# Performance work log

Hardware: AMD Instinct MI355X
Metric: run time of the kernel (lower is better)

The kernel has to match this reference:

```python
import jax, jax.numpy as jnp
import numpy as np

N, C_IN, H, W = 32, 16, 256, 256
C_OUT, K = 64, 3

def setup_inputs() -> dict:
    key = jax.random.key(0)
    kx, kw, kb = jax.random.split(key, 3)
    x = jax.random.normal(kx, (N, C_IN, H, W), dtype=jnp.float32)
    # PyTorch Conv2d default init: U(-b, b), b = 1/sqrt(fan_in)
    bound = 1.0 / np.sqrt(C_IN * K * K)
    conv_weight = jax.random.uniform(kw, (C_OUT, C_IN, K, K), minval=-bound, maxval=bound, dtype=jnp.float32)
    conv_bias = jax.random.uniform(kb, (C_OUT,), minval=-bound, maxval=bound, dtype=jnp.float32)
    return {"x": x, "conv_weight": conv_weight, "conv_bias": conv_bias}

def reference(x, conv_weight, conv_bias):
    # conv2d, stride=1, padding=0 (VALID), NCHW / OIHW
    y = jax.lax.conv_general_dilated(
        x, conv_weight,
        window_strides=(1, 1), padding="VALID",
        dimension_numbers=("NCHW", "OIHW", "NCHW"))
    y = y + conv_bias[None, :, None, None]
    # min over output channels (keepdim -> 1 channel), then double tanh
    y = jnp.min(y, axis=1, keepdims=True)  # [N,1,OH,OW]
    return jnp.tanh(jnp.tanh(y))
```

## Files before the change

kernel.cpp:

```cpp
#include <hip/hip_runtime.h>

typedef __bf16 bf16x8 __attribute__((ext_vector_type(8)));
typedef unsigned short us8 __attribute__((ext_vector_type(8)));
typedef unsigned short us2 __attribute__((ext_vector_type(2)));
typedef float f32x16 __attribute__((ext_vector_type(16)));

#define N_IMG 32
#define CI 16
#define HH 256
#define WW 256
#define CO 64
#define OHH 254
#define OWW 254
#define RPB 2
#define NBLK_H (OHH / RPB)
#define NBLK (N_IMG * NBLK_H)

#define XS_W 258
#define XS_C 24
#define WP_SHORTS (CO * 160)
#define WS_NEEDED ((size_t)WP_SHORTS * 2)

__device__ __forceinline__ unsigned short f2bf(float f) {
  union { float f; unsigned u; } v; v.f = f;
  return (unsigned short)((v.u + 0x7FFFu + ((v.u >> 16) & 1u)) >> 16);
}

#if defined(__has_builtin)
#if __has_builtin(__builtin_amdgcn_cvt_pk_bf16_f32)
#define HAVE_CVT_PK 1
#endif
#endif

__device__ __forceinline__ us2 cvt2(float a, float b) {
#ifdef HAVE_CVT_PK
  typedef __bf16 bf16x2 __attribute__((ext_vector_type(2)));
  bf16x2 r = __builtin_amdgcn_cvt_pk_bf16_f32(a, b);
  return __builtin_bit_cast(us2, r);
#else
  us2 r; r[0] = f2bf(a); r[1] = f2bf(b); return r;
#endif
}

__device__ __forceinline__ float fast_tanh(float x) {
  float cx = fminf(fmaxf(x, -15.f), 15.f);
  float e = __expf(2.f * cx);
  return (e - 1.f) / (e + 1.f);
}

__global__ void prep_w(const float* __restrict__ wg, const float* __restrict__ bg,
                       unsigned short* __restrict__ wp) {
  int idx = blockIdx.x * 256 + threadIdx.x;
  if (idx >= WP_SHORTS) return;
  int oc = idx / 160;
  int k = idx - oc * 160;
  int tap = k >> 4, ci = k & 15;
  float v;
  if (tap < 9)      v = wg[oc * 144 + ci * 9 + tap];
  else if (ci == 0) v = bg[oc];
  else              v = 0.f;
  wp[idx] = f2bf(v);
}

__global__ __launch_bounds__(256, 3)
void conv_fused(const float* __restrict__ xg, const unsigned short* __restrict__ wp,
                float* __restrict__ out) {
  __shared__ __align__(16) unsigned short xs[(RPB + 2) * XS_W * XS_C];
  const int t = threadIdx.x;
  const int n = blockIdx.x / NBLK_H;
  const int oh0 = (blockIdx.x - n * NBLK_H) * RPB;

  {
    const float* src = xg + (size_t)n * (CI * HH * WW) + t;
    float v[RPB + 2][16];
#pragma unroll
    for (int r = 0; r < RPB + 2; ++r)
#pragma unroll
      for (int j = 0; j < 16; ++j)
        v[r][j] = src[((size_t)j * HH + (oh0 + r)) * WW];
#pragma unroll
    for (int r = 0; r < RPB + 2; ++r) {
      union { us8 v8[2]; us2 v2[8]; } pk;
#pragma unroll
      for (int j = 0; j < 8; ++j) pk.v2[j] = cvt2(v[r][2 * j], v[r][2 * j + 1]);
      *(us8*)(xs + (r * XS_W + t) * XS_C) = pk.v8[0];
      *(us8*)(xs + (r * XS_W + t) * XS_C + 8) = pk.v8[1];
    }
  }
  if (t < 32 * (RPB + 2)) {
    int r = t >> 5, rem = t & 31;
    int w = 256 + (rem >> 4), ci = rem & 15;
    xs[(r * XS_W + w) * XS_C + ci] = 0;
  }
  __syncthreads();

  const int lane = t & 63, wave = t >> 6;
  const int lr = lane & 31, qh = lane >> 5;

  const unsigned short* wpl = wp + lr * 160 + qh * 8;
  bf16x8 afrag[2][10];
#pragma unroll
  for (int mt = 0; mt < 2; ++mt)
#pragma unroll
    for (int tap = 0; tap < 10; ++tap)
      afrag[mt][tap] =
          __builtin_bit_cast(bf16x8, *(const us8*)(wpl + mt * 32 * 160 + tap * 16));

  us8 onev = {};
  if (qh == 0) onev[0] = 0x3F80;
  const bf16x8 xone = __builtin_bit_cast(bf16x8, onev);

  const int pb = wave * 64;

#pragma unroll
  for (int r = 0; r < RPB; ++r) {
    f32x16 acc[2][2];
#pragma unroll
    for (int a = 0; a < 2; ++a)
#pragma unroll
      for (int b = 0; b < 2; ++b)
#pragma unroll
        for (int e = 0; e < 16; ++e) acc[a][b][e] = 0.f;

#pragma unroll
    for (int tap = 0; tap < 9; ++tap) {
      const int kh = tap / 3, kw = tap - kh * 3;
#pragma unroll
      for (int nt = 0; nt < 2; ++nt) {
        bf16x8 xf = __builtin_bit_cast(
            bf16x8,
            *(const us8*)(xs + ((r + kh) * XS_W + pb + nt * 32 + lr + kw) * XS_C +
                          qh * 8));
        acc[0][nt] = __builtin_amdgcn_mfma_f32_32x32x16_bf16(afrag[0][tap], xf,
                                                             acc[0][nt], 0, 0, 0);
        acc[1][nt] = __builtin_amdgcn_mfma_f32_32x32x16_bf16(afrag[1][tap], xf,
                                                             acc[1][nt], 0, 0, 0);
      }
    }
#pragma unroll
    for (int nt = 0; nt < 2; ++nt) {
      acc[0][nt] = __builtin_amdgcn_mfma_f32_32x32x16_bf16(afrag[0][9], xone,
                                                           acc[0][nt], 0, 0, 0);
      acc[1][nt] = __builtin_amdgcn_mfma_f32_32x32x16_bf16(afrag[1][9], xone,
                                                           acc[1][nt], 0, 0, 0);
    }

    float vmin[2];
#pragma unroll
    for (int nt = 0; nt < 2; ++nt) {
      float v = acc[0][nt][0];
#pragma unroll
      for (int e = 1; e < 16; ++e) v = fminf(v, acc[0][nt][e]);
#pragma unroll
      for (int e = 0; e < 16; ++e) v = fminf(v, acc[1][nt][e]);
      v = fminf(v, __shfl_xor(v, 32, 64));
      vmin[nt] = fast_tanh(fast_tanh(v));
    }
    float res = (lane < 32) ? vmin[0] : vmin[1];
    int ow = pb + lane;
    if (ow < OWW) out[((size_t)n * OHH + (oh0 + r)) * OWW + ow] = res;
  }
}

#define WS_K 168
__global__ __launch_bounds__(256, 2)
void conv_min_tanh(const float* __restrict__ xg, const float* __restrict__ wg,
                   const float* __restrict__ bg, float* __restrict__ out) {
  __shared__ __align__(16) unsigned short xs[3 * XS_W * XS_C];
  __shared__ __align__(16) unsigned short ws[CO * WS_K];
  const int t = threadIdx.x;
  const int n = blockIdx.x / OHH;
  const int oh = blockIdx.x % OHH;
#pragma unroll
  for (int i = 0; i < 36; ++i) {
    int f = i * 256 + t;
    int oc = f / 144;
    int r = f - oc * 144;
    int ci = r / 9;
    int tap = r - ci * 9;
    ws[oc * WS_K + tap * 16 + ci] = f2bf(wg[f]);
  }
  if (t < CO) ws[t * WS_K + 144] = f2bf(bg[t]);
  for (int i = t; i < CO * 15; i += 256) {
    int oc = i / 15;
    ws[oc * WS_K + 145 + (i - oc * 15)] = 0;
  }
  {
    const size_t base_n = (size_t)n * CI * HH * WW;
#pragma unroll
    for (int kh = 0; kh < 3; ++kh) {
#pragma unroll
      for (int half = 0; half < 2; ++half) {
        float v[8];
#pragma unroll
        for (int j = 0; j < 8; ++j) {
          int ci = half * 8 + j;
          v[j] = xg[base_n + ((size_t)ci * HH + (oh + kh)) * WW + t];
        }
        us8 pk;
#pragma unroll
        for (int j = 0; j < 8; ++j) pk[j] = f2bf(v[j]);
        *(us8*)(xs + (kh * XS_W + t) * XS_C + half * 8) = pk;
      }
    }
  }
  if (t < 96) {
    int kh = t >> 5;
    int rem = t & 31;
    int w = 256 + (rem >> 4);
    int ci = rem & 15;
    xs[(kh * XS_W + w) * XS_C + ci] = 0;
  }
  __syncthreads();
  const int lane = t & 63, wave = t >> 6;
  const int lr = lane & 31, qh = lane >> 5;
  bf16x8 afrag[2][10];
#pragma unroll
  for (int mt = 0; mt < 2; ++mt) {
    const unsigned short* wq = ws + (mt * 32 + lr) * WS_K + qh * 8;
#pragma unroll
    for (int tap = 0; tap < 10; ++tap)
      afrag[mt][tap] = __builtin_bit_cast(bf16x8, *(const us8*)(wq + tap * 16));
  }
  f32x16 acc[2][2];
#pragma unroll
  for (int a = 0; a < 2; ++a)
#pragma unroll
    for (int b = 0; b < 2; ++b)
#pragma unroll
      for (int e = 0; e < 16; ++e) acc[a][b][e] = 0.f;
  const unsigned short* xq = xs + (wave * 64 + lr) * XS_C + qh * 8;
#pragma unroll
  for (int tap = 0; tap < 9; ++tap) {
    const int kh = tap / 3, kw = tap - kh * 3;
#pragma unroll
    for (int nt = 0; nt < 2; ++nt) {
      bf16x8 xf = __builtin_bit_cast(
          bf16x8, *(const us8*)(xq + (kh * XS_W + nt * 32 + kw) * XS_C));
      acc[0][nt] = __builtin_amdgcn_mfma_f32_32x32x16_bf16(afrag[0][tap], xf,
                                                           acc[0][nt], 0, 0, 0);
      acc[1][nt] = __builtin_amdgcn_mfma_f32_32x32x16_bf16(afrag[1][tap], xf,
                                                           acc[1][nt], 0, 0, 0);
    }
  }
  {
    us8 one = {};
    if (qh == 0) one[0] = 0x3F80;
    bf16x8 xone = __builtin_bit_cast(bf16x8, one);
#pragma unroll
    for (int nt = 0; nt < 2; ++nt) {
      acc[0][nt] = __builtin_amdgcn_mfma_f32_32x32x16_bf16(afrag[0][9], xone,
                                                           acc[0][nt], 0, 0, 0);
      acc[1][nt] = __builtin_amdgcn_mfma_f32_32x32x16_bf16(afrag[1][9], xone,
                                                           acc[1][nt], 0, 0, 0);
    }
  }
  float vmin[2];
#pragma unroll
  for (int nt = 0; nt < 2; ++nt) {
    float v = acc[0][nt][0];
#pragma unroll
    for (int e = 1; e < 16; ++e) v = fminf(v, acc[0][nt][e]);
#pragma unroll
    for (int e = 0; e < 16; ++e) v = fminf(v, acc[1][nt][e]);
    v = fminf(v, __shfl_xor(v, 32, 64));
    vmin[nt] = fast_tanh(fast_tanh(v));
  }
  float res = (lane < 32) ? vmin[0] : vmin[1];
  int ow = wave * 64 + lane;
  if (ow < OWW) out[((size_t)n * OHH + oh) * OWW + ow] = res;
}

extern "C" void kernel_launch(void* const* d_in, const int* in_sizes, int n_in,
                              void* d_out, int out_size, void* d_ws, size_t ws_size,
                              hipStream_t stream) {
  const float* x = (const float*)d_in[0];
  const float* w = (const float*)d_in[1];
  const float* b = (const float*)d_in[2];
  float* out = (float*)d_out;
  if (ws_size >= WS_NEEDED) {
    unsigned short* wp = (unsigned short*)d_ws;
    prep_w<<<dim3((WP_SHORTS + 255) / 256), dim3(256), 0, stream>>>(w, b, wp);
    conv_fused<<<dim3(NBLK), dim3(256), 0, stream>>>(x, wp, out);
  } else {
    conv_min_tanh<<<dim3(N_IMG * OHH), dim3(256), 0, stream>>>(x, w, b, out);
  }
}
```

Measured before the change: 213.3 us.

## Stream row strips through a 4-slot ring buffer with prefetched input rows

Each block now covers a strip of 10-11 output rows instead of 2, so each input row is loaded and converted about once rather than being re-staged up to twice (RPB=2 blocks stage 4 rows for 2 output rows). Rows live in a 4-slot circular LDS buffer, and the next row's global loads are issued before the MFMA work and written back after it, overlapping load latency with compute. The LDS channel stride drops from 24 to 16 shorts, which cuts LDS use but may add bank conflicts. The grid shrinks to 768 blocks, which leaves less parallelism and adds a barrier per row.

Result: faster. 208.2 us (-2.4%).

```diff
diff --git a/kernel.cpp b/kernel.cpp
--- a/kernel.cpp
+++ b/kernel.cpp
@@ -12,12 +12,10 @@
 #define CO 64
 #define OHH 254
 #define OWW 254
-#define RPB 2
-#define NBLK_H (OHH / RPB)
-#define NBLK (N_IMG * NBLK_H)
 
 #define XS_W 258
-#define XS_C 24
+#define SC 16
+#define NSTRIP 24
 #define WP_SHORTS (CO * 160)
 #define WS_NEEDED ((size_t)WP_SHORTS * 2)
 
@@ -65,34 +63,37 @@
 __global__ __launch_bounds__(256, 3)
 void conv_fused(const float* __restrict__ xg, const unsigned short* __restrict__ wp,
                 float* __restrict__ out) {
-  __shared__ __align__(16) unsigned short xs[(RPB + 2) * XS_W * XS_C];
+  __shared__ __align__(16) unsigned short xs[4 * XS_W * SC];
   const int t = threadIdx.x;
-  const int n = blockIdx.x / NBLK_H;
-  const int oh0 = (blockIdx.x - n * NBLK_H) * RPB;
+  const int n = blockIdx.x / NSTRIP;
+  const int s = blockIdx.x - n * NSTRIP;
+  const int oh0 = s * 10 + (s < 14 ? s : 14);
+  const int nrows = (s < 14) ? 11 : 10;
+  const int oh1 = oh0 + nrows;
+
+  const float* srcT = xg + (size_t)n * (CI * HH * WW) + t;
 
   {
-    const float* src = xg + (size_t)n * (CI * HH * WW) + t;
-    float v[RPB + 2][16];
-#pragma unroll
-    for (int r = 0; r < RPB + 2; ++r)
+    float v[3][16];
+#pragma unroll
+    for (int r = 0; r < 3; ++r)
 #pragma unroll
       for (int j = 0; j < 16; ++j)
-        v[r][j] = src[((size_t)j * HH + (oh0 + r)) * WW];
-#pragma unroll
-    for (int r = 0; r < RPB + 2; ++r) {
+        v[r][j] = srcT[((size_t)j * HH + (oh0 + r)) * WW];
+#pragma unroll
+    for (int r = 0; r < 3; ++r) {
       union { us8 v8[2]; us2 v2[8]; } pk;
 #pragma unroll
       for (int j = 0; j < 8; ++j) pk.v2[j] = cvt2(v[r][2 * j], v[r][2 * j + 1]);
-      *(us8*)(xs + (r * XS_W + t) * XS_C) = pk.v8[0];
-      *(us8*)(xs + (r * XS_W + t) * XS_C + 8) = pk.v8[1];
-    }
-  }
-  if (t < 32 * (RPB + 2)) {
-    int r = t >> 5, rem = t & 31;
-    int w = 256 + (rem >> 4), ci = rem & 15;
-    xs[(r * XS_W + w) * XS_C + ci] = 0;
-  }
-  __syncthreads();
+      const int slot = (oh0 + r) & 3;
+      *(us8*)(xs + (slot * XS_W + t) * SC) = pk.v8[0];
+      *(us8*)(xs + (slot * XS_W + t) * SC + 8) = pk.v8[1];
+    }
+  }
+  if (t < 128) {
+    const int slot = t >> 5, rem = t & 31;
+    xs[(slot * XS_W + 256 + (rem >> 4)) * SC + (rem & 15)] = 0;
+  }
 
   const int lane = t & 63, wave = t >> 6;
   const int lr = lane & 31, qh = lane >> 5;
@@ -112,56 +113,64 @@
 
   const int pb = wave * 64;
 
-#pragma unroll
-  for (int r = 0; r < RPB; ++r) {
-    f32x16 acc[2][2];
-#pragma unroll
-    for (int a = 0; a < 2; ++a)
-#pragma unroll
-      for (int b = 0; b < 2; ++b)
-#pragma unroll
-        for (int e = 0; e < 16; ++e) acc[a][b][e] = 0.f;
-
-#pragma unroll
-    for (int tap = 0; tap < 9; ++tap) {
-      const int kh = tap / 3, kw = tap - kh * 3;
-#pragma unroll
-      for (int nt = 0; nt < 2; ++nt) {
+  __syncthreads();
+
+  for (int oh = oh0; oh < oh1; ++oh) {
+    const bool do_stage = (oh + 1 < oh1);
+
+    float v[16];
+    if (do_stage) {
+#pragma unroll
+      for (int j = 0; j < 16; ++j)
+        v[j] = srcT[((size_t)j * HH + (oh + 3)) * WW];
+    }
+
+    float vmin[2];
+#pragma unroll
+    for (int nt = 0; nt < 2; ++nt) {
+      f32x16 acc0, acc1;
+#pragma unroll
+      for (int e = 0; e < 16; ++e) { acc0[e] = 0.f; acc1[e] = 0.f; }
+#pragma unroll
+      for (int tap = 0; tap < 9; ++tap) {
+        const int kh = tap / 3, kw = tap - kh * 3;
+        const int slot = (oh + kh) & 3;
         bf16x8 xf = __builtin_bit_cast(
             bf16x8,
-            *(const us8*)(xs + ((r + kh) * XS_W + pb + nt * 32 + lr + kw) * XS_C +
-                          qh * 8));
-        acc[0][nt] = __builtin_amdgcn_mfma_f32_32x32x16_bf16(afrag[0][tap], xf,
-                                                             acc[0][nt], 0, 0, 0);
-        acc[1][nt] = __builtin_amdgcn_mfma_f32_32x32x16_bf16(afrag[1][tap], xf,
-                                                             acc[1][nt], 0, 0, 0);
+            *(const us8*)(xs + (slot * XS_W + pb + nt * 32 + lr + kw) * SC + qh * 8));
+        acc0 = __builtin_amdgcn_mfma_f32_32x32x16_bf16(afrag[0][tap], xf, acc0, 0, 0, 0);
+        acc1 = __builtin_amdgcn_mfma_f32_32x32x16_bf16(afrag[1][tap], xf, acc1, 0, 0, 0);
       }
-    }
-#pragma unroll
-    for (int nt = 0; nt < 2; ++nt) {
-      acc[0][nt] = __builtin_amdgcn_mfma_f32_32x32x16_bf16(afrag[0][9], xone,
-                                                           acc[0][nt], 0, 0, 0);
-      acc[1][nt] = __builtin_amdgcn_mfma_f32_32x32x16_bf16(afrag[1][9], xone,
-                                                           acc[1][nt], 0, 0, 0);
-    }
-
-    float vmin[2];
-#pragma unroll
-    for (int nt = 0; nt < 2; ++nt) {
-      float v = acc[0][nt][0];
-#pragma unroll
-      for (int e = 1; e < 16; ++e) v = fminf(v, acc[0][nt][e]);
-#pragma unroll
-      for (int e = 0; e < 16; ++e) v = fminf(v, acc[1][nt][e]);
-      v = fminf(v, __shfl_xor(v, 32, 64));
-      vmin[nt] = fast_tanh(fast_tanh(v));
-    }
-    float res = (lane < 32) ? vmin[0] : vmin[1];
-    int ow = pb + lane;
-    if (ow < OWW) out[((size_t)n * OHH + (oh0 + r)) * OWW + ow] = res;
-  }
-}
-
+      acc0 = __builtin_amdgcn_mfma_f32_32x32x16_bf16(afrag[0][9], xone, acc0, 0, 0, 0);
+      acc1 = __builtin_amdgcn_mfma_f32_32x32x16_bf16(afrag[1][9], xone, acc1, 0, 0, 0);
+
+      float mv = acc0[0];
+#pragma unroll
+      for (int e = 1; e < 16; ++e) mv = fminf(mv, acc0[e]);
+#pragma unroll
+      for (int e = 0; e < 16; ++e) mv = fminf(mv, acc1[e]);
+      mv = fminf(mv, __shfl_xor(mv, 32, 64));
+      vmin[nt] = fast_tanh(fast_tanh(mv));
+    }
+
+    if (do_stage) {
+      union { us8 v8[2]; us2 v2[8]; } pk;
+#pragma unroll
+      for (int j = 0; j < 8; ++j) pk.v2[j] = cvt2(v[2 * j], v[2 * j + 1]);
+      const int slot = (oh + 3) & 3;
+      *(us8*)(xs + (slot * XS_W + t) * SC) = pk.v8[0];
+      *(us8*)(xs + (slot * XS_W + t) * SC + 8) = pk.v8[1];
+    }
+
+    const float res = (lane < 32) ? vmin[0] : vmin[1];
+    const int ow = pb + lane;
+    if (ow < OWW) out[((size_t)n * OHH + oh) * OWW + ow] = res;
+
+    __syncthreads();
+  }
+}
+
+#define XS_C 24
 #define WS_K 168
 __global__ __launch_bounds__(256, 2)
 void conv_min_tanh(const float* __restrict__ xg, const float* __restrict__ wg,
@@ -281,7 +290,7 @@
   if (ws_size >= WS_NEEDED) {
     unsigned short* wp = (unsigned short*)d_ws;
     prep_w<<<dim3((WP_SHORTS + 255) / 256), dim3(256), 0, stream>>>(w, b, wp);
-    conv_fused<<<dim3(NBLK), dim3(256), 0, stream>>>(x, wp, out);
+    conv_fused<<<dim3(N_IMG * NSTRIP), dim3(256), 0, stream>>>(x, wp, out);
   } else {
     conv_min_tanh<<<dim3(N_IMG * OHH), dim3(256), 0, stream>>>(x, w, b, out);
   }
```
